# Kernel tuning notes

Hardware: AMD Instinct MI355X
Metric: run time of the kernel (lower is better)

## Reference

```python
import jax, jax.numpy as jnp
import numpy as np

D_MODEL = 256
N_LAYER = 4
D_INNER = 512   # expand=2
D_STATE = 16
DT_RANK = 16    # ceil(d_model/16)
D_CONV = 4
VOCAB = 16
BATCH = 1
SEQLEN = 4096
EPS = 1e-5


def setup_inputs() -> dict:
    key = jax.random.key(0)
    ks = jax.random.split(key, 10)
    s = 0.02
    A_init = jnp.log(jnp.arange(1, D_STATE + 1, dtype=jnp.float32))  # S4D-real init
    return {
        "input_ids": jax.random.randint(ks[0], (BATCH, SEQLEN), 0, VOCAB, dtype=jnp.int32),
        "embed_w": jax.random.normal(ks[1], (VOCAB, D_MODEL), jnp.float32) * s,
        "norm_w": jnp.ones((N_LAYER, D_MODEL), jnp.float32),
        "in_proj_w": jax.random.normal(ks[2], (N_LAYER, 2 * D_INNER, D_MODEL), jnp.float32) * s,
        "out_proj_w": jax.random.normal(ks[3], (N_LAYER, D_MODEL, D_INNER), jnp.float32) * s,
        "conv_w": jax.random.normal(ks[4], (N_LAYER, 2, D_INNER, D_CONV), jnp.float32) * s,
        "conv_b": jnp.zeros((N_LAYER, 2, D_INNER), jnp.float32),
        "x_proj_w": jax.random.normal(ks[5], (N_LAYER, 2, DT_RANK + 2 * D_STATE, D_INNER), jnp.float32) * s,
        "dt_proj_w": jax.random.normal(ks[6], (N_LAYER, 2, D_INNER, DT_RANK), jnp.float32) * s,
        "dt_proj_b": jax.random.normal(ks[7], (N_LAYER, 2, D_INNER), jnp.float32) * 0.1,
        "A_log": jnp.broadcast_to(A_init, (N_LAYER, 2, D_INNER, D_STATE)) + 0.0,
        "Dp": jnp.ones((N_LAYER, 2, D_INNER), jnp.float32),
        "norm_f_w": jnp.ones((D_MODEL,), jnp.float32),
    }


def rmsnorm(x, w):
    return x * jax.lax.rsqrt(jnp.mean(x * x, axis=-1, keepdims=True) + EPS) * w


def selective_scan(u, dt, A, Bm, Cm, Dv):
    # u, dt: (B,L,Di); A: (Di,N); Bm, Cm: (B,L,N); Dv: (Di,)
    dA = jnp.exp(dt[..., None] * A)                         # (B,L,Di,N)
    dBu = dt[..., None] * Bm[:, :, None, :] * u[..., None]  # (B,L,Di,N)

    def step(h, xs):
        dA_t, dBu_t, C_t = xs
        h = dA_t * h + dBu_t                                # (B,Di,N)
        y = jnp.einsum('bdn,bn->bd', h, C_t)
        return h, y

    h0 = jnp.zeros((u.shape[0], D_INNER, D_STATE), u.dtype)
    xs = (jnp.moveaxis(dA, 1, 0), jnp.moveaxis(dBu, 1, 0), jnp.moveaxis(Cm, 1, 0))
    _, ys = jax.lax.scan(step, h0, xs)                      # (L,B,Di)
    return jnp.moveaxis(ys, 0, 1) + u * Dv


def mamba_dir(x, in_w, out_w, cw, cb, xpw, dtw, dtb, a_log, dv):
    # x: (B,L,D)
    xz = jnp.einsum('bld,ed->ble', x, in_w)                 # (B,L,2*Di)
    u, z = jnp.split(xz, 2, axis=-1)
    # causal depthwise conv1d
    uc = jnp.moveaxis(u, 1, 2)                              # (B,Di,L)
    uc = jax.lax.conv_general_dilated(
        uc, cw[:, None, :], (1,), [(D_CONV - 1, 0)],
        feature_group_count=D_INNER, dimension_numbers=('NCH', 'OIH', 'NCH'))
    u = jax.nn.silu(jnp.moveaxis(uc, 1, 2) + cb)            # (B,L,Di)
    xdb = jnp.einsum('bld,ed->ble', u, xpw)                 # (B,L,dt_rank+2N)
    dt_r, Bm, Cm = jnp.split(xdb, [DT_RANK, DT_RANK + D_STATE], axis=-1)
    dt = jax.nn.softplus(jnp.einsum('blr,dr->bld', dt_r, dtw) + dtb)
    A = -jnp.exp(a_log)                                     # (Di,N)
    y = selective_scan(u, dt, A, Bm, Cm, dv)
    y = y * jax.nn.silu(z)
    return jnp.einsum('bld,od->blo', y, out_w)


def reference(input_ids, embed_w, norm_w, in_proj_w, out_proj_w, conv_w, conv_b,
              x_proj_w, dt_proj_w, dt_proj_b, A_log, Dp, norm_f_w):
    h = embed_w[input_ids]                                  # (B,L,D)
    residual = None
    for i in range(N_LAYER):
        residual = h if residual is None else h + residual  # residual_in_fp32
        hn = rmsnorm(residual, norm_w[i])
        out_f = mamba_dir(hn, in_proj_w[i], out_proj_w[i], conv_w[i, 0], conv_b[i, 0],
                          x_proj_w[i, 0], dt_proj_w[i, 0], dt_proj_b[i, 0], A_log[i, 0], Dp[i, 0])
        out_r = mamba_dir(hn[:, ::-1], in_proj_w[i], out_proj_w[i], conv_w[i, 1], conv_b[i, 1],
                          x_proj_w[i, 1], dt_proj_w[i, 1], dt_proj_b[i, 1], A_log[i, 1], Dp[i, 1])[:, ::-1]
        h = out_f + out_r                                   # bidirectional 'add'
    residual = h + residual
    return rmsnorm(residual, norm_f_w)
```

## Files before the change

kernel.cpp:

```cpp
#include <hip/hip_runtime.h>
#include <hip/hip_bf16.h>
#include <math.h>

#define L_  4096
#define D_  256
#define DI_ 512
#define NS_ 16
#define NC_ 128
#define CH_ 32

typedef __attribute__((ext_vector_type(8))) short short8;
typedef __attribute__((ext_vector_type(4))) short short4v;
typedef __attribute__((ext_vector_type(4))) float f32x4;

__global__ __launch_bounds__(256) void prep_kernel(const int* __restrict__ ids,
    const float* __restrict__ ew, const float* __restrict__ inw,
    const float* __restrict__ outw, const float* __restrict__ xpw,
    float* __restrict__ res, __hip_bfloat16* __restrict__ inw_b,
    __hip_bfloat16* __restrict__ outw_b, __hip_bfloat16* __restrict__ xpw_b) {
  int idx = blockIdx.x * 256 + threadIdx.x;
  int l = idx >> 8, d = idx & 255;
  res[idx] = ew[ids[l] * D_ + d];
  inw_b[idx] = __float2bfloat16(inw[idx]);
  {
    int layer = idx >> 18;
    int rem = idx & 262143;
    int o = rem >> 10, k = rem & 1023;
    outw_b[idx] = __float2bfloat16(outw[((size_t)layer * 256 + o) * 512 + (k & 511)]);
  }
  if (idx < 4 * 2 * 64 * 512) {
    int layer = idx >> 16;
    int rem = idx & 65535;
    int dir = rem >> 15;
    int r = (rem >> 9) & 63, k = idx & 511;
    float v = (r < 48) ? xpw[(((size_t)layer * 2 + dir) * 48 + r) * 512 + k] : 0.f;
    xpw_b[idx] = __float2bfloat16(v);
  }
}

template<bool BF16OUT>
__global__ __launch_bounds__(256) void rmsnorm_kernel(float* __restrict__ residual,
    const float* __restrict__ hadd, const float* __restrict__ w, void* __restrict__ out) {
  int row = blockIdx.x * 4 + (threadIdx.x >> 6);
  int lane = threadIdx.x & 63;
  size_t o = (size_t)row * D_ + lane * 4;
  float4 v = *(const float4*)(residual + o);
  if (hadd) {
    float4 a = *(const float4*)(hadd + o);
    v.x += a.x; v.y += a.y; v.z += a.z; v.w += a.w;
    *(float4*)(residual + o) = v;
  }
  float sq = fmaf(v.x, v.x, fmaf(v.y, v.y, fmaf(v.z, v.z, v.w * v.w)));
  #pragma unroll
  for (int s = 32; s > 0; s >>= 1) sq += __shfl_xor(sq, s, 64);
  float scale = rsqrtf(sq * (1.f / D_) + 1e-5f);
  float4 wv = *(const float4*)(w + lane * 4);
  float r0 = v.x * scale * wv.x, r1 = v.y * scale * wv.y;
  float r2 = v.z * scale * wv.z, r3 = v.w * scale * wv.w;
  if (BF16OUT) {
    __hip_bfloat16* ob = (__hip_bfloat16*)out + o;
    short4v s4;
    s4[0] = __bfloat16_as_short(__float2bfloat16(r0));
    s4[1] = __bfloat16_as_short(__float2bfloat16(r1));
    s4[2] = __bfloat16_as_short(__float2bfloat16(r2));
    s4[3] = __bfloat16_as_short(__float2bfloat16(r3));
    *reinterpret_cast<short4v*>(ob) = s4;
  } else {
    float4 r = {r0, r1, r2, r3};
    *((float4*)out + (o >> 2)) = r;
  }
}

__device__ __forceinline__ void gload_lds16(const void* g, void* l) {
  __builtin_amdgcn_global_load_lds((const __attribute__((address_space(1))) unsigned int*)g,
                                   (__attribute__((address_space(3))) unsigned int*)l,
                                   16, 0, 0);
}

template<int BM, int BN, bool BF16OUT>
__global__ __launch_bounds__(256) void gemm_bt_bf16(const __hip_bfloat16* __restrict__ A,
    const __hip_bfloat16* __restrict__ B, void* __restrict__ Cv, int M, int N, int K,
    size_t sA, size_t sB, size_t sC) {
  A += (size_t)blockIdx.z * sA; B += (size_t)blockIdx.z * sB;
  constexpr int FM = (BM / 2) / 16, FN = (BN / 2) / 16;
  constexpr int ABYTES = BM * 64, BBYTES = BN * 64;
  __shared__ __attribute__((aligned(16))) char As[ABYTES];
  __shared__ __attribute__((aligned(16))) char Bs[BBYTES];
  int tid = threadIdx.x, lane = tid & 63, w = tid >> 6;
  int bm = blockIdx.y * BM, bn = blockIdx.x * BN;
  int wr = (w >> 1) * (BM / 2), wc = (w & 1) * (BN / 2);
  f32x4 acc[FM][FN] = {};
  for (int k0 = 0; k0 < K; k0 += 32) {
    __syncthreads();
    #pragma unroll
    for (int i = 0; i < ABYTES / 4096; ++i) {
      int x = (i * 256 + tid) * 16;
      int xs = x ^ (((x >> 7) & 3) << 4);
      int row = xs >> 6, col = (xs & 63) >> 1;
      gload_lds16(A + (size_t)(bm + row) * K + k0 + col, As + i * 4096 + w * 1024);
    }
    #pragma unroll
    for (int i = 0; i < BBYTES / 4096; ++i) {
      int x = (i * 256 + tid) * 16;
      int xs = x ^ (((x >> 7) & 3) << 4);
      int row = xs >> 6, col = (xs & 63) >> 1;
      gload_lds16(B + (size_t)(bn + row) * K + k0 + col, Bs + i * 4096 + w * 1024);
    }
    __syncthreads();
    short8 af[FM], bf[FN];
    #pragma unroll
    for (int m = 0; m < FM; ++m) {
      int row = wr + m * 16 + (lane & 15);
      int x = row * 64 + ((lane >> 4) * 16);
      x ^= ((x >> 7) & 3) << 4;
      af[m] = *reinterpret_cast<const short8*>(As + x);
    }
    #pragma unroll
    for (int n = 0; n < FN; ++n) {
      int row = wc + n * 16 + (lane & 15);
      int x = row * 64 + ((lane >> 4) * 16);
      x ^= ((x >> 7) & 3) << 4;
      bf[n] = *reinterpret_cast<const short8*>(Bs + x);
    }
    #pragma unroll
    for (int m = 0; m < FM; ++m)
      #pragma unroll
      for (int n = 0; n < FN; ++n)
        acc[m][n] = __builtin_amdgcn_mfma_f32_16x16x32_bf16(af[m], bf[n], acc[m][n], 0, 0, 0);
  }
  #pragma unroll
  for (int m = 0; m < FM; ++m)
    #pragma unroll
    for (int n = 0; n < FN; ++n)
      #pragma unroll
      for (int j = 0; j < 4; ++j) {
        size_t off = (size_t)blockIdx.z * sC +
                     (size_t)(bm + wr + m * 16 + (lane >> 4) * 4 + j) * N + bn + wc + n * 16 + (lane & 15);
        if (BF16OUT) ((__hip_bfloat16*)Cv)[off] = __float2bfloat16(acc[m][n][j]);
        else         ((float*)Cv)[off] = acc[m][n][j];
      }
}

__global__ __launch_bounds__(256) void xproj_conv(const __hip_bfloat16* __restrict__ xz,
    const float* __restrict__ cw, const float* __restrict__ cb,
    const __hip_bfloat16* __restrict__ xpw_b, float* __restrict__ xdb,
    __hip_bfloat16* __restrict__ ucb) {
  int dir = blockIdx.y;
  int l0 = blockIdx.x * 32;
  int tid = threadIdx.x, lane = tid & 63, w = tid >> 6;
  __shared__ __attribute__((aligned(16))) unsigned short sxz[36][512];
  __shared__ __attribute__((aligned(16))) unsigned short su[32][520];
  __shared__ __attribute__((aligned(16))) char Bs[4096];
  #pragma unroll
  for (int it = 0; it < 9; ++it) {
    int s = it * 4 + w;
    int sc = s > 34 ? 34 : s;
    int f = l0 - 3 + sc;
    int row = dir ? (L_ - 1 - f) : f;
    row = row < 0 ? 0 : (row > L_ - 1 ? L_ - 1 : row);
    gload_lds16((const char*)xz + (size_t)row * 2048 + lane * 16, (char*)sxz + s * 1024);
  }
  __syncthreads();
  unsigned short* ucs = (unsigned short*)ucb;
  #pragma unroll
  for (int half = 0; half < 2; ++half) {
    int ch = half * 256 + tid;
    float4 wv = *(const float4*)(cw + ((size_t)dir * DI_ + ch) * 4);
    float bias = cb[(size_t)dir * DI_ + ch];
    #pragma unroll 4
    for (int t = 0; t < 32; ++t) {
      float acc = bias;
      #pragma unroll
      for (int k = 0; k < 4; ++k) {
        float xv = (l0 == 0 && t + k < 3) ? 0.f
                 : __uint_as_float((unsigned)sxz[t + k][ch] << 16);
        acc = fmaf(((const float*)&wv)[k], xv, acc);
      }
      float uvf = acc * __builtin_amdgcn_rcpf(1.f + __expf(-acc));
      unsigned short bits = (unsigned short)__bfloat16_as_short(__float2bfloat16(uvf));
      su[t][ch] = bits;
      ucs[((size_t)dir * L_ + l0 + t) * DI_ + ch] = bits;
    }
  }
  const __hip_bfloat16* B = xpw_b + (size_t)dir * 64 * 512;
  int wr = (w >> 1) * 16, wc = (w & 1) * 32;
  f32x4 acc2[2] = {};
  for (int k0 = 0; k0 < 512; k0 += 32) {
    __syncthreads();
    {
      int x = tid * 16;
      int xs = x ^ (((x >> 7) & 3) << 4);
      int row = xs >> 6, col = (xs & 63) >> 1;
      gload_lds16(B + (size_t)row * 512 + k0 + col, Bs + w * 1024);
    }
    __syncthreads();
    short8 af = *reinterpret_cast<const short8*>(
        (const char*)su + (wr + (lane & 15)) * 1040 + (k0 + (lane >> 4) * 8) * 2);
    #pragma unroll
    for (int n = 0; n < 2; ++n) {
      int row = wc + n * 16 + (lane & 15);
      int x = row * 64 + ((lane >> 4) * 16);
      x ^= ((x >> 7) & 3) << 4;
      short8 bf8 = *reinterpret_cast<const short8*>(Bs + x);
      acc2[n] = __builtin_amdgcn_mfma_f32_16x16x32_bf16(af, bf8, acc2[n], 0, 0, 0);
    }
  }
  #pragma unroll
  for (int n = 0; n < 2; ++n)
    #pragma unroll
    for (int j = 0; j < 4; ++j)
      xdb[((size_t)dir * L_ + l0 + wr + (lane >> 4) * 4 + j) * 64 + wc + n * 16 + (lane & 15)]
          = acc2[n][j];
}

__device__ __forceinline__ void scan_stage3(int tid, int lane, int w, int q, int dir, int c,
    const float* __restrict__ xdb, const __hip_bfloat16* __restrict__ uc,
    const float* __restrict__ dtw, const float* __restrict__ dtbp,
    float (*sxdb)[64], unsigned short (*su)[128], float (*sdt)[128]) {
  const char* bg = (const char*)(xdb + ((size_t)dir * L_ + (size_t)c * CH_) * 64);
  const char* ug = (const char*)(uc + ((size_t)dir * L_ + (size_t)c * CH_) * DI_ + q * 128);
  #pragma unroll
  for (int i = 0; i < 2; ++i)
    gload_lds16(bg + w * 2048 + i * 1024 + lane * 16, (char*)sxdb + w * 2048 + i * 1024);
  #pragma unroll
  for (int i = 0; i < 2; ++i) {
    int byte = (w * 128 + i * 64 + lane) * 16;
    gload_lds16(ug + (byte >> 8) * 1024 + (byte & 255), (char*)su + w * 2048 + i * 1024);
  }
  __syncthreads();
  int dlx = tid & 127, tst = tid >> 7;
  int dc = q * 128 + dlx;
  const float4* wr = (const float4*)(dtw + ((size_t)dir * DI_ + dc) * 16);
  float4 w0 = wr[0], w1 = wr[1], w2 = wr[2], w3 = wr[3];
  float bias = dtbp[(size_t)dir * DI_ + dc];
  #pragma unroll
  for (int i = 0; i < 16; ++i) {
    int t = tst + i * 2;
    const float4* xr = (const float4*)&sxdb[t][0];
    float4 x0 = xr[0], x1 = xr[1], x2 = xr[2], x3 = xr[3];
    float acc = bias;
    acc = fmaf(w0.x, x0.x, fmaf(w0.y, x0.y, fmaf(w0.z, x0.z, fmaf(w0.w, x0.w, acc))));
    acc = fmaf(w1.x, x1.x, fmaf(w1.y, x1.y, fmaf(w1.z, x1.z, fmaf(w1.w, x1.w, acc))));
    acc = fmaf(w2.x, x2.x, fmaf(w2.y, x2.y, fmaf(w2.z, x2.z, fmaf(w2.w, x2.w, acc))));
    acc = fmaf(w3.x, x3.x, fmaf(w3.y, x3.y, fmaf(w3.z, x3.z, fmaf(w3.w, x3.w, acc))));
    float e = __expf(fminf(acc, 20.f));
    sdt[t][dlx] = acc > 20.f ? acc : __logf(1.f + e);
  }
  __syncthreads();
}

__global__ __launch_bounds__(256) void scan_pass1(const __hip_bfloat16* __restrict__ uc,
    const float* __restrict__ xdb, const float* __restrict__ dtw,
    const float* __restrict__ dtbp, const float* __restrict__ A_log,
    float* __restrict__ Pb, float* __restrict__ Qb) {
  int dir = blockIdx.y;
  int c = blockIdx.x >> 2, q = blockIdx.x & 3;
  int tid = threadIdx.x, lane = tid & 63, w = tid >> 6;
  int dl = tid >> 1, nh = tid & 1;
  int d = q * 128 + dl;
  __shared__ __attribute__((aligned(16))) float sxdb[CH_][64];
  __shared__ __attribute__((aligned(16))) unsigned short su[CH_][128];
  __shared__ __attribute__((aligned(16))) float sdt[CH_][128];
  float Av[8], P[8], Q[8];
  const float4* Ab4 = (const float4*)(A_log + ((size_t)dir * DI_ + d) * 16 + nh * 8);
  float4 a0 = Ab4[0], a1 = Ab4[1];
  float al[8] = {a0.x, a0.y, a0.z, a0.w, a1.x, a1.y, a1.z, a1.w};
  #pragma unroll
  for (int j = 0; j < 8; ++j) { Av[j] = -__expf(al[j]); P[j] = 1.f; Q[j] = 0.f; }
  scan_stage3(tid, lane, w, q, dir, c, xdb, uc, dtw, dtbp, sxdb, su, sdt);
  #pragma unroll 2
  for (int t = 0; t < CH_; ++t) {
    float dtv = sdt[t][dl];
    float uv  = __uint_as_float((unsigned)su[t][dl] << 16);
    float du = dtv * uv;
    const float4* Br = (const float4*)&sxdb[t][16 + nh * 8];
    float4 b0 = Br[0], b1 = Br[1];
    float bb[8] = {b0.x, b0.y, b0.z, b0.w, b1.x, b1.y, b1.z, b1.w};
    #pragma unroll
    for (int j = 0; j < 8; ++j) {
      float dA = __expf(dtv * Av[j]);
      P[j] *= dA;
      Q[j] = fmaf(dA, Q[j], bb[j] * du);
    }
  }
  size_t ob = ((size_t)dir * NC_ + c) * 8192 + (size_t)(nh * 8) * 512 + d;
  #pragma unroll
  for (int j = 0; j < 8; ++j) { Pb[ob + j * 512] = P[j]; Qb[ob + j * 512] = Q[j]; }
}

__global__ __launch_bounds__(64) void scan_combine(const float* __restrict__ Pb,
    const float* __restrict__ Qb, float* __restrict__ H0) {
  int idx = blockIdx.x * 64 + threadIdx.x;
  int dir = idx >> 13; int s = idx & 8191;
  size_t base = (size_t)dir * NC_ * 8192 + s;
  float h = 0.f;
  #pragma unroll 8
  for (int c = 0; c < NC_; ++c) {
    size_t o = base + (size_t)c * 8192;
    H0[o] = h;
    h = fmaf(Pb[o], h, Qb[o]);
  }
}

__global__ __launch_bounds__(256) void scan_pass2(const __hip_bfloat16* __restrict__ uc,
    const float* __restrict__ xdb, const float* __restrict__ dtw,
    const float* __restrict__ dtbp, const float* __restrict__ A_log,
    const float* __restrict__ Dp, const __hip_bfloat16* __restrict__ xz,
    const float* __restrict__ H0, __hip_bfloat16* __restrict__ yg) {
  int dir = blockIdx.y;
  int c = blockIdx.x >> 2, q = blockIdx.x & 3;
  int tid = threadIdx.x, lane = tid & 63, w = tid >> 6;
  int dl = tid >> 1, nh = tid & 1;
  int d = q * 128 + dl;
  __shared__ __attribute__((aligned(16))) float sxdb[CH_][64];
  __shared__ __attribute__((aligned(16))) unsigned short su[CH_][128];
  __shared__ __attribute__((aligned(16))) float sdt[CH_][128];
  float Av[8], h[8];
  const float4* Ab4 = (const float4*)(A_log + ((size_t)dir * DI_ + d) * 16 + nh * 8);
  float4 a0 = Ab4[0], a1 = Ab4[1];
  float al[8] = {a0.x, a0.y, a0.z, a0.w, a1.x, a1.y, a1.z, a1.w};
  size_t ob = ((size_t)dir * NC_ + c) * 8192 + (size_t)(nh * 8) * 512 + d;
  #pragma unroll
  for (int j = 0; j < 8; ++j) { Av[j] = -__expf(al[j]); h[j] = H0[ob + j * 512]; }
  float Dv = Dp[(size_t)dir * DI_ + d];
  scan_stage3(tid, lane, w, q, dir, c, xdb, uc, dtw, dtbp, sxdb, su, sdt);
  #pragma unroll 2
  for (int t = 0; t < CH_; ++t) {
    float dtv = sdt[t][dl];
    float uv  = __uint_as_float((unsigned)su[t][dl] << 16);
    float du = dtv * uv;
    const float4* Br = (const float4*)&sxdb[t][16 + nh * 8];
    const float4* Cr = (const float4*)&sxdb[t][32 + nh * 8];
    float4 b0 = Br[0], b1 = Br[1], c0 = Cr[0], c1 = Cr[1];
    float bb[8] = {b0.x, b0.y, b0.z, b0.w, b1.x, b1.y, b1.z, b1.w};
    float cc[8] = {c0.x, c0.y, c0.z, c0.w, c1.x, c1.y, c1.z, c1.w};
    float y = 0.f;
    #pragma unroll
    for (int j = 0; j < 8; ++j) {
      float dA = __expf(dtv * Av[j]);
      h[j] = fmaf(dA, h[j], bb[j] * du);
      y = fmaf(h[j], cc[j], y);
    }
    y += __shfl_xor(y, 1, 64);
    if (nh == 0) {
      int l = c * CH_ + t;
      int pos = dir ? (L_ - 1 - l) : l;
      float zv = __bfloat162float(xz[(size_t)pos * 1024 + DI_ + d]);
      float g = zv * __builtin_amdgcn_rcpf(1.f + __expf(-zv));
      yg[(size_t)pos * 1024 + (size_t)dir * DI_ + d] = __float2bfloat16((y + uv * Dv) * g);
    }
  }
}

extern "C" void kernel_launch(void* const* d_in, const int* in_sizes, int n_in,
                              void* d_out, int out_size, void* d_ws, size_t ws_size,
                              hipStream_t stream) {
  const int*   ids       = (const int*)  d_in[0];
  const float* embed_w   = (const float*)d_in[1];
  const float* norm_w    = (const float*)d_in[2];
  const float* in_proj_w = (const float*)d_in[3];
  const float* out_proj_w= (const float*)d_in[4];
  const float* conv_w    = (const float*)d_in[5];
  const float* conv_b    = (const float*)d_in[6];
  const float* x_proj_w  = (const float*)d_in[7];
  const float* dt_proj_w = (const float*)d_in[8];
  const float* dt_proj_b = (const float*)d_in[9];
  const float* A_log     = (const float*)d_in[10];
  const float* Dp        = (const float*)d_in[11];
  const float* norm_f_w  = (const float*)d_in[12];

  float* ws = (float*)d_ws;
  float* residual = ws; ws += (size_t)L_ * D_;
  float* xdb      = ws; ws += (size_t)2 * L_ * 64;
  float* hbuf     = ws; ws += (size_t)L_ * D_;
  float* Pb       = ws; ws += (size_t)2 * NC_ * 8192;
  float* Qb       = ws; ws += (size_t)2 * NC_ * 8192;
  float* H0       = ws; ws += (size_t)2 * NC_ * 8192;
  __hip_bfloat16* hn_b   = (__hip_bfloat16*)ws;
  __hip_bfloat16* xz_b   = hn_b + (size_t)L_ * D_;
  __hip_bfloat16* yg_b   = xz_b + (size_t)L_ * 1024;
  __hip_bfloat16* uc_b   = yg_b + (size_t)L_ * 1024;
  __hip_bfloat16* inw_b  = uc_b + (size_t)2 * L_ * DI_;
  __hip_bfloat16* outw_b = inw_b + (size_t)4 * 1024 * D_;
  __hip_bfloat16* xpw_b  = outw_b + (size_t)4 * D_ * 1024;

  prep_kernel<<<L_ * D_ / 256, 256, 0, stream>>>(ids, embed_w, in_proj_w, out_proj_w,
                                                 x_proj_w, residual, inw_b, outw_b, xpw_b);

  for (int i = 0; i < 4; ++i) {
    rmsnorm_kernel<true><<<L_ / 4, 256, 0, stream>>>(residual, i ? hbuf : nullptr,
                                                     norm_w + (size_t)i * D_, hn_b);
    gemm_bt_bf16<128, 64, true><<<dim3(1024 / 64, L_ / 128, 1), 256, 0, stream>>>(
        hn_b, inw_b + (size_t)i * 1024 * D_, xz_b, L_, 1024, D_, 0, 0, 0);
    xproj_conv<<<dim3(L_ / 32, 2), 256, 0, stream>>>(
        xz_b, conv_w + (size_t)i * 2 * DI_ * 4, conv_b + (size_t)i * 2 * DI_,
        xpw_b + (size_t)i * 2 * 64 * DI_, xdb, uc_b);
    dim3 gsc(NC_ * 4, 2);
    scan_pass1<<<gsc, 256, 0, stream>>>(
        uc_b, xdb, dt_proj_w + (size_t)i * 2 * DI_ * 16, dt_proj_b + (size_t)i * 2 * DI_,
        A_log + (size_t)i * 2 * DI_ * NS_, Pb, Qb);
    scan_combine<<<256, 64, 0, stream>>>(Pb, Qb, H0);
    scan_pass2<<<gsc, 256, 0, stream>>>(
        uc_b, xdb, dt_proj_w + (size_t)i * 2 * DI_ * 16, dt_proj_b + (size_t)i * 2 * DI_,
        A_log + (size_t)i * 2 * DI_ * NS_, Dp + (size_t)i * 2 * DI_,
        xz_b, H0, yg_b);
    gemm_bt_bf16<64, 64, false><<<dim3(D_ / 64, L_ / 64, 1), 256, 0, stream>>>(
        yg_b, outw_b + (size_t)i * D_ * 1024, hbuf, L_, D_, 1024, 0, 0, 0);
  }

  rmsnorm_kernel<false><<<L_ / 4, 256, 0, stream>>>(residual, hbuf, norm_f_w, d_out);
}
```

Before: 436.4 us.

## Split sequential chunk-state combine into three-level segmented scan

Replaces the single combine kernel, where each of 16384 chains walks all 128 chunks serially over 256 small blocks, with a three-phase segmented scan. Segment aggregates are computed in parallel over 8 segments, a short serial scan runs across the segments, then the segments are expanded in parallel. This exposes 8x more parallelism to hide memory latency on the serial chain. The cost is two extra kernel launches per layer and an extra read of Pb/Qb.

```diff
diff --git a/kernel.cpp b/kernel.cpp
--- a/kernel.cpp
+++ b/kernel.cpp
@@ -288,15 +288,46 @@
   for (int j = 0; j < 8; ++j) { Pb[ob + j * 512] = P[j]; Qb[ob + j * 512] = Q[j]; }
 }
 
-__global__ __launch_bounds__(64) void scan_combine(const float* __restrict__ Pb,
-    const float* __restrict__ Qb, float* __restrict__ H0) {
-  int idx = blockIdx.x * 64 + threadIdx.x;
-  int dir = idx >> 13; int s = idx & 8191;
+__global__ __launch_bounds__(256) void combine_a(const float* __restrict__ Pb,
+    const float* __restrict__ Qb, float* __restrict__ Pseg, float* __restrict__ Qseg) {
+  int chain = blockIdx.x * 256 + threadIdx.x;
+  int seg = blockIdx.y;
+  int dir = chain >> 13, s = chain & 8191;
   size_t base = (size_t)dir * NC_ * 8192 + s;
+  float P = 1.f, Q = 0.f;
+  #pragma unroll 16
+  for (int cc = 0; cc < 16; ++cc) {
+    size_t o = base + (size_t)(seg * 16 + cc) * 8192;
+    float p = Pb[o], q = Qb[o];
+    Q = fmaf(p, Q, q);
+    P *= p;
+  }
+  Pseg[seg * 16384 + chain] = P;
+  Qseg[seg * 16384 + chain] = Q;
+}
+
+__global__ __launch_bounds__(256) void combine_b(const float* __restrict__ Pseg,
+    const float* __restrict__ Qseg, float* __restrict__ Hseg) {
+  int chain = blockIdx.x * 256 + threadIdx.x;
   float h = 0.f;
-  #pragma unroll 8
-  for (int c = 0; c < NC_; ++c) {
-    size_t o = base + (size_t)c * 8192;
+  #pragma unroll
+  for (int seg = 0; seg < 8; ++seg) {
+    Hseg[seg * 16384 + chain] = h;
+    h = fmaf(Pseg[seg * 16384 + chain], h, Qseg[seg * 16384 + chain]);
+  }
+}
+
+__global__ __launch_bounds__(256) void combine_c(const float* __restrict__ Pb,
+    const float* __restrict__ Qb, const float* __restrict__ Hseg,
+    float* __restrict__ H0) {
+  int chain = blockIdx.x * 256 + threadIdx.x;
+  int seg = blockIdx.y;
+  int dir = chain >> 13, s = chain & 8191;
+  size_t base = (size_t)dir * NC_ * 8192 + s;
+  float h = Hseg[seg * 16384 + chain];
+  #pragma unroll 16
+  for (int cc = 0; cc < 16; ++cc) {
+    size_t o = base + (size_t)(seg * 16 + cc) * 8192;
     H0[o] = h;
     h = fmaf(Pb[o], h, Qb[o]);
   }
@@ -376,6 +407,9 @@
   float* Pb       = ws; ws += (size_t)2 * NC_ * 8192;
   float* Qb       = ws; ws += (size_t)2 * NC_ * 8192;
   float* H0       = ws; ws += (size_t)2 * NC_ * 8192;
+  float* Pseg     = ws; ws += (size_t)8 * 16384;
+  float* Qseg     = ws; ws += (size_t)8 * 16384;
+  float* Hseg     = ws; ws += (size_t)8 * 16384;
   __hip_bfloat16* hn_b   = (__hip_bfloat16*)ws;
   __hip_bfloat16* xz_b   = hn_b + (size_t)L_ * D_;
   __hip_bfloat16* yg_b   = xz_b + (size_t)L_ * 1024;
@@ -399,7 +433,9 @@
     scan_pass1<<<gsc, 256, 0, stream>>>(
         uc_b, xdb, dt_proj_w + (size_t)i * 2 * DI_ * 16, dt_proj_b + (size_t)i * 2 * DI_,
         A_log + (size_t)i * 2 * DI_ * NS_, Pb, Qb);
-    scan_combine<<<256, 64, 0, stream>>>(Pb, Qb, H0);
+    combine_a<<<dim3(64, 8), 256, 0, stream>>>(Pb, Qb, Pseg, Qseg);
+    combine_b<<<64, 256, 0, stream>>>(Pseg, Qseg, Hseg);
+    combine_c<<<dim3(64, 8), 256, 0, stream>>>(Pb, Qb, Hseg, H0);
     scan_pass2<<<gsc, 256, 0, stream>>>(
         uc_b, xdb, dt_proj_w + (size_t)i * 2 * DI_ * 16, dt_proj_b + (size_t)i * 2 * DI_,
         A_log + (size_t)i * 2 * DI_ * NS_, Dp + (size_t)i * 2 * DI_,
```

Result: no change. 435.6 us, median of 2 (-0.2%).
